# Kernel tuning notes

Measured on AMD Instinct MI355X. Metric: run time of the kernel, lower is better.

Reference implementation:

```python
import jax, jax.numpy as jnp
import numpy as np

N, L = 1, 384
NODE, H, PD = 256, 8, 128
HD = NODE // H
D1 = H * PD + NODE  # out_transform input dim = 1280


def instance_norm(x, eps=1e-5):
    # x: (N, C, H, W); torch InstanceNorm2d default: no affine, biased var
    m = x.mean(axis=(2, 3), keepdims=True)
    v = x.var(axis=(2, 3), keepdims=True)
    return (x - m) / jnp.sqrt(v + eps)


def conv3x3(x, w, b):
    y = jax.lax.conv_general_dilated(x, w, (1, 1), 'SAME',
                                     dimension_numbers=('NCHW', 'OIHW', 'NCHW'))
    return y + b[None, :, None, None]


def leaky(x):
    return jnp.where(x >= 0, x, 0.01 * x)


def layer_norm(x, w, b, eps=1e-5):
    m = x.mean(-1, keepdims=True)
    v = x.var(-1, keepdims=True)
    return (x - m) / jnp.sqrt(v + eps) * w + b


def setup_inputs() -> dict:
    key = jax.random.key(0)
    ks = jax.random.split(key, 32)
    s = 0.05
    inp = {
        'x': jax.random.normal(ks[0], (N, L, NODE), jnp.float32),
        'z': jax.random.normal(ks[1], (N, L, L, PD), jnp.float32),
        'plddt': jax.random.uniform(ks[2], (N, L, L, 1), jnp.float32),
        # linear weights stored (in, out) so application is x @ W
        'Wq': jax.random.normal(ks[3], (NODE, NODE), jnp.float32) * s,
        'Wk': jax.random.normal(ks[4], (NODE, NODE), jnp.float32) * s,
        'Wv': jax.random.normal(ks[5], (NODE, NODE), jnp.float32) * s,
        'Wp2a': jax.random.normal(ks[6], (PD, H), jnp.float32) * s,
        'conv_a_w': jax.random.normal(ks[7], (H, 2 * H, 3, 3), jnp.float32) * s,
        'conv_a_b': jnp.zeros((H,), jnp.float32),
        'conv_m_w': jax.random.normal(ks[8], (H, H + 1, 3, 3), jnp.float32) * s,
        'conv_m_b': jnp.zeros((H,), jnp.float32),
        'ln1_w': jnp.ones((D1,), jnp.float32),
        'ln1_b': jnp.zeros((D1,), jnp.float32),
        'lin1_w': jax.random.normal(ks[9], (D1, 2 * NODE), jnp.float32) * s,
        'lin1_b': jnp.zeros((2 * NODE,), jnp.float32),
        'ln2_w': jnp.ones((2 * NODE,), jnp.float32),
        'ln2_b': jnp.zeros((2 * NODE,), jnp.float32),
        'lin2_w': jax.random.normal(ks[10], (2 * NODE, NODE), jnp.float32) * s,
        'lin2_b': jnp.zeros((NODE,), jnp.float32),
        'lnf_w': jnp.ones((NODE,), jnp.float32),
        'lnf_b': jnp.zeros((NODE,), jnp.float32),
        'conv_p_w': jax.random.normal(ks[11], (PD, H + PD, 3, 3), jnp.float32) * s,
        'conv_p_b': jnp.zeros((PD,), jnp.float32),
    }
    return inp


def reference(x, z, plddt, Wq, Wk, Wv, Wp2a, conv_a_w, conv_a_b, conv_m_w,
              conv_m_b, ln1_w, ln1_b, lin1_w, lin1_b, ln2_w, ln2_b, lin2_w,
              lin2_b, lnf_w, lnf_b, conv_p_w, conv_p_b):
    Nb, Lh, D = x.shape
    nh = conv_a_w.shape[0]
    hd = D // nh
    Pd = z.shape[-1]
    # node -> alpha (GAT-style QK scores per head)
    q = (x @ Wq).reshape(Nb, Lh, nh, hd)
    k = (x @ Wk).reshape(Nb, Lh, nh, hd)
    v = (x @ Wv).reshape(Nb, Lh, nh, hd)
    a_node = jnp.einsum('nlhd,nmhd->nlmh', q, k) / jnp.sqrt(jnp.float32(hd))
    a_pair = z @ Wp2a                                  # (N,L,L,H)
    a = jnp.concatenate([a_pair, a_node], -1).transpose(0, 3, 1, 2)  # (N,2H,L,L)
    a = leaky(conv3x3(instance_norm(a), conv_a_w, conv_a_b))
    a = jnp.concatenate([a, plddt.transpose(0, 3, 1, 2)], 1)          # (N,H+1,L,L)
    a = leaky(conv3x3(instance_norm(a), conv_m_w, conv_m_b))
    a = a.transpose(0, 2, 3, 1)                                        # (N,L,L,H)
    # aggregations
    nfn = jnp.einsum('nlmh,nmhd->nlhd', a, v).reshape(Nb, Lh, D)       # node from node
    nfp = jnp.einsum('nlmh,nlmp->nlhp', a, z).reshape(Nb, Lh, nh * Pd) # node from pair
    cat = jnp.concatenate([nfp, nfn], -1)
    h = layer_norm(cat, ln1_w, ln1_b) @ lin1_w + lin1_b
    h = leaky(layer_norm(h, ln2_w, ln2_b)) @ lin2_w + lin2_b
    x_new = layer_norm(x + h, lnf_w, lnf_b)
    zp = jnp.concatenate([z, a], -1).transpose(0, 3, 1, 2)             # (N,P+H,L,L)
    z_new = leaky(conv3x3(instance_norm(zp), conv_p_w, conv_p_b)).transpose(0, 2, 3, 1)
    return x_new, z_new
```

## Files before the change

kernel.cpp:

```cpp
#include <hip/hip_runtime.h>
#include <stdint.h>

#define LSEQ 384
#define LL   147456
#define NODE 256
#define NH   8
#define HD   32
#define PDIM 128
#define D1   1280
#define D2   512

typedef __attribute__((ext_vector_type(8))) short s16x8;
typedef __attribute__((ext_vector_type(8))) __bf16 bf16x8;
typedef __attribute__((ext_vector_type(4))) float f32x4;

__device__ __forceinline__ float bf2f(uint16_t u) {
    union { uint32_t i; float f; } x; x.i = ((uint32_t)u) << 16; return x.f;
}
__device__ __forceinline__ uint16_t f2bf(float f) {
    uint32_t b = __float_as_uint(f);
    return (uint16_t)((b + 0x7FFFu + ((b >> 16) & 1u)) >> 16);
}
__device__ __forceinline__ float ld(const void* p, size_t i, int bf) {
    return bf ? bf2f(((const uint16_t*)p)[i]) : ((const float*)p)[i];
}
__device__ __forceinline__ void stout(void* p, size_t i, float v, int bf) {
    if (bf) ((uint16_t*)p)[i] = f2bf(v);
    else    ((float*)p)[i] = v;
}

__device__ __forceinline__ bf16x8 bf16x8_zero() {
    union { s16x8 s; bf16x8 b; } u; u.s = (s16x8)0; return u.b;
}

__device__ __forceinline__ void block_reduce2_256(float* s1, float* s2, int t) {
    __syncthreads();
    for (int o = 128; o > 0; o >>= 1) {
        if (t < o) { s1[t] += s1[t + o]; s2[t] += s2[t + o]; }
        __syncthreads();
    }
}

__device__ __forceinline__ void acc8(uint4 u, float& s, float& ss) {
    uint32_t w[4] = { u.x, u.y, u.z, u.w };
    #pragma unroll
    for (int i = 0; i < 4; ++i) {
        float a = bf2f((uint16_t)(w[i] & 0xFFFFu));
        float b = bf2f((uint16_t)(w[i] >> 16));
        s += a + b;
        ss = fmaf(a, a, ss);
        ss = fmaf(b, b, ss);
    }
}

__global__ void k_detect(const uint32_t* __restrict__ zz, int* __restrict__ flag) {
    if (threadIdx.x == 0 && blockIdx.x == 0) {
        int cnt = 0;
        for (int i = 0; i < 256; ++i) {
            uint32_t lo = zz[i] & 0xFFFFu;
            uint32_t e = (lo >> 7) & 0xFFu;
            if (lo == 0u || (e >= 96u && e <= 142u)) ++cnt;
        }
        flag[0] = (cnt >= 192) ? 1 : 0;
    }
}

__global__ __launch_bounds__(256) void k_cvt(
    const void* __restrict__ src, uint16_t* __restrict__ dst, const int* __restrict__ dt)
{
    int bf = dt[0];
    int i = blockIdx.x * 256 + threadIdx.x;
    dst[i] = f2bf(ld(src, i, bf));
}

__global__ __launch_bounds__(256) void k_wnk(
    const void* __restrict__ src, uint16_t* __restrict__ dst, int K, int N,
    const int* __restrict__ dt)
{
    __shared__ float tile[32][33];
    int bf = dt[0];
    int k0 = blockIdx.x * 32, n0 = blockIdx.y * 32;
    int tr = threadIdx.x >> 5, tc = threadIdx.x & 31;
    #pragma unroll
    for (int i = 0; i < 4; ++i)
        tile[tr + i * 8][tc] = ld(src, (size_t)(k0 + tr + i * 8) * N + n0 + tc, bf);
    __syncthreads();
    #pragma unroll
    for (int i = 0; i < 4; ++i)
        dst[(size_t)(n0 + tr + i * 8) * K + k0 + tc] = f2bf(tile[tc][tr + i * 8]);
}

__global__ __launch_bounds__(256) void k_gemm_bias_f32(
    const uint16_t* __restrict__ A, const uint16_t* __restrict__ B,
    const void* __restrict__ bias, float* __restrict__ out, int K, int N,
    const int* __restrict__ dt)
{
    __shared__ __align__(16) uint16_t As[64 * 72];
    __shared__ __align__(16) uint16_t Bs[64 * 72];
    int bf = dt[0];
    int t = threadIdx.x;
    int row0 = blockIdx.x * 64, col0 = blockIdx.y * 64;
    int w = t >> 6, lane = t & 63, p = lane & 15, g = lane >> 4;
    int wm = w >> 1, wn = w & 1;
    f32x4 acc[2][2];
    #pragma unroll
    for (int i = 0; i < 2; ++i)
        #pragma unroll
        for (int j = 0; j < 2; ++j) acc[i][j] = (f32x4){0.f, 0.f, 0.f, 0.f};

    for (int kc = 0; kc < K; kc += 64) {
        __syncthreads();
        #pragma unroll
        for (int rep = 0; rep < 2; ++rep) {
            int i = t + rep * 256;
            int r = i >> 3, c8 = (i & 7) * 8;
            *(uint4*)&As[r * 72 + c8] = *(const uint4*)&A[(size_t)(row0 + r) * K + kc + c8];
            *(uint4*)&Bs[r * 72 + c8] = *(const uint4*)&B[(size_t)(col0 + r) * K + kc + c8];
        }
        __syncthreads();
        #pragma unroll
        for (int kk = 0; kk < 64; kk += 32) {
            bf16x8 a0 = *(const bf16x8*)&As[(wm * 32 + p) * 72 + kk + 8 * g];
            bf16x8 a1 = *(const bf16x8*)&As[(wm * 32 + 16 + p) * 72 + kk + 8 * g];
            bf16x8 b0 = *(const bf16x8*)&Bs[(wn * 32 + p) * 72 + kk + 8 * g];
            bf16x8 b1 = *(const bf16x8*)&Bs[(wn * 32 + 16 + p) * 72 + kk + 8 * g];
            acc[0][0] = __builtin_amdgcn_mfma_f32_16x16x32_bf16(a0, b0, acc[0][0], 0, 0, 0);
            acc[0][1] = __builtin_amdgcn_mfma_f32_16x16x32_bf16(a0, b1, acc[0][1], 0, 0, 0);
            acc[1][0] = __builtin_amdgcn_mfma_f32_16x16x32_bf16(a1, b0, acc[1][0], 0, 0, 0);
            acc[1][1] = __builtin_amdgcn_mfma_f32_16x16x32_bf16(a1, b1, acc[1][1], 0, 0, 0);
        }
    }
    #pragma unroll
    for (int mi = 0; mi < 2; ++mi)
        #pragma unroll
        for (int ni = 0; ni < 2; ++ni) {
            int n = col0 + wn * 32 + ni * 16 + p;
            float bb = ld(bias, n, bf);
            #pragma unroll
            for (int reg = 0; reg < 4; ++reg) {
                int m = row0 + wm * 32 + mi * 16 + 4 * g + reg;
                out[(size_t)m * N + n] = acc[mi][ni][reg] + bb;
            }
        }
}

__global__ __launch_bounds__(256) void k_gemm_qkv(
    const uint16_t* __restrict__ A, const uint16_t* __restrict__ B,
    uint16_t* __restrict__ q, uint16_t* __restrict__ k, uint16_t* __restrict__ v)
{
    __shared__ __align__(16) uint16_t As[64 * 72];
    __shared__ __align__(16) uint16_t Bs[64 * 72];
    const int K = 256;
    int t = threadIdx.x;
    int row0 = blockIdx.x * 64, col0 = blockIdx.y * 64;
    int w = t >> 6, lane = t & 63, p = lane & 15, g = lane >> 4;
    int wm = w >> 1, wn = w & 1;
    f32x4 acc[2][2];
    #pragma unroll
    for (int i = 0; i < 2; ++i)
        #pragma unroll
        for (int j = 0; j < 2; ++j) acc[i][j] = (f32x4){0.f, 0.f, 0.f, 0.f};

    for (int kc = 0; kc < K; kc += 64) {
        __syncthreads();
        #pragma unroll
        for (int rep = 0; rep < 2; ++rep) {
            int i = t + rep * 256;
            int r = i >> 3, c8 = (i & 7) * 8;
            *(uint4*)&As[r * 72 + c8] = *(const uint4*)&A[(size_t)(row0 + r) * K + kc + c8];
            *(uint4*)&Bs[r * 72 + c8] = *(const uint4*)&B[(size_t)(col0 + r) * K + kc + c8];
        }
        __syncthreads();
        #pragma unroll
        for (int kk = 0; kk < 64; kk += 32) {
            bf16x8 a0 = *(const bf16x8*)&As[(wm * 32 + p) * 72 + kk + 8 * g];
            bf16x8 a1 = *(const bf16x8*)&As[(wm * 32 + 16 + p) * 72 + kk + 8 * g];
            bf16x8 b0 = *(const bf16x8*)&Bs[(wn * 32 + p) * 72 + kk + 8 * g];
            bf16x8 b1 = *(const bf16x8*)&Bs[(wn * 32 + 16 + p) * 72 + kk + 8 * g];
            acc[0][0] = __builtin_amdgcn_mfma_f32_16x16x32_bf16(a0, b0, acc[0][0], 0, 0, 0);
            acc[0][1] = __builtin_amdgcn_mfma_f32_16x16x32_bf16(a0, b1, acc[0][1], 0, 0, 0);
            acc[1][0] = __builtin_amdgcn_mfma_f32_16x16x32_bf16(a1, b0, acc[1][0], 0, 0, 0);
            acc[1][1] = __builtin_amdgcn_mfma_f32_16x16x32_bf16(a1, b1, acc[1][1], 0, 0, 0);
        }
    }
    #pragma unroll
    for (int mi = 0; mi < 2; ++mi)
        #pragma unroll
        for (int ni = 0; ni < 2; ++ni) {
            int nglob = col0 + wn * 32 + ni * 16 + p;
            int sel = nglob >> 8, col = nglob & 255;
            uint16_t* dst = (sel == 0) ? q : (sel == 1) ? k : v;
            #pragma unroll
            for (int reg = 0; reg < 4; ++reg) {
                int m = row0 + wm * 32 + mi * 16 + 4 * g + reg;
                dst[(size_t)m * 256 + col] = f2bf(acc[mi][ni][reg]);
            }
        }
}

__global__ __launch_bounds__(256) void k_lin2lnf_mfma(
    const uint16_t* __restrict__ A, const uint16_t* __restrict__ B,
    const void* __restrict__ bias, const void* __restrict__ x,
    const void* __restrict__ lnw, const void* __restrict__ lnb,
    void* __restrict__ out, const int* __restrict__ dt)
{
    __shared__ __align__(16) uint16_t As[32 * 72];
    __shared__ __align__(16) uint16_t Bs[256 * 72];
    const int K = 512;
    int bf = dt[0];
    int t = threadIdx.x;
    int row0 = blockIdx.x * 32;
    int w = t >> 6, lane = t & 63, p = lane & 15, g = lane >> 4;
    f32x4 acc[2][4];
    #pragma unroll
    for (int i = 0; i < 2; ++i)
        #pragma unroll
        for (int j = 0; j < 4; ++j) acc[i][j] = (f32x4){0.f, 0.f, 0.f, 0.f};

    for (int kc = 0; kc < K; kc += 64) {
        __syncthreads();
        {
            int r = t >> 3, c8 = (t & 7) * 8;
            *(uint4*)&As[r * 72 + c8] = *(const uint4*)&A[(size_t)(row0 + r) * K + kc + c8];
        }
        #pragma unroll
        for (int rep = 0; rep < 8; ++rep) {
            int i = t + rep * 256;
            int r = i >> 3, c8 = (i & 7) * 8;
            *(uint4*)&Bs[r * 72 + c8] = *(const uint4*)&B[(size_t)r * K + kc + c8];
        }
        __syncthreads();
        #pragma unroll
        for (int kk = 0; kk < 64; kk += 32) {
            bf16x8 a0 = *(const bf16x8*)&As[(p) * 72 + kk + 8 * g];
            bf16x8 a1 = *(const bf16x8*)&As[(16 + p) * 72 + kk + 8 * g];
            #pragma unroll
            for (int ni = 0; ni < 4; ++ni) {
                bf16x8 bq = *(const bf16x8*)&Bs[(w * 64 + ni * 16 + p) * 72 + kk + 8 * g];
                acc[0][ni] = __builtin_amdgcn_mfma_f32_16x16x32_bf16(a0, bq, acc[0][ni], 0, 0, 0);
                acc[1][ni] = __builtin_amdgcn_mfma_f32_16x16x32_bf16(a1, bq, acc[1][ni], 0, 0, 0);
            }
        }
    }
    __syncthreads();
    float* lnt = (float*)Bs;
    #pragma unroll
    for (int mi = 0; mi < 2; ++mi)
        #pragma unroll
        for (int ni = 0; ni < 4; ++ni) {
            int n = w * 64 + ni * 16 + p;
            float bb = ld(bias, n, bf);
            #pragma unroll
            for (int reg = 0; reg < 4; ++reg) {
                int m = mi * 16 + 4 * g + reg;
                lnt[m * 264 + n] = acc[mi][ni][reg] + bb + ld(x, (size_t)(row0 + m) * 256 + n, bf);
            }
        }
    __syncthreads();
    for (int rr = 0; rr < 8; ++rr) {
        int m = w * 8 + rr;
        float4 v4 = *(const float4*)&lnt[m * 264 + lane * 4];
        float vv[4] = { v4.x, v4.y, v4.z, v4.w };
        float s = (vv[0] + vv[1]) + (vv[2] + vv[3]);
        float ss = fmaf(vv[0], vv[0], fmaf(vv[1], vv[1], fmaf(vv[2], vv[2], vv[3] * vv[3])));
        #pragma unroll
        for (int off = 32; off > 0; off >>= 1) {
            s  += __shfl_xor(s, off);
            ss += __shfl_xor(ss, off);
        }
        float mean = s / 256.f;
        float rstd = rsqrtf(fmaxf(ss / 256.f - mean * mean, 0.f) + 1e-5f);
        #pragma unroll
        for (int i = 0; i < 4; ++i) {
            int c = lane * 4 + i;
            float val = (vv[i] - mean) * rstd * ld(lnw, c, bf) + ld(lnb, c, bf);
            stout(out, (size_t)(row0 + m) * 256 + c, val, bf);
        }
    }
}

__global__ __launch_bounds__(256) void k_apair(
    const void* __restrict__ z, const void* __restrict__ Wp2a,
    uint16_t* __restrict__ acat, const int* __restrict__ dt)
{
    __shared__ float zl[32 * 129];
    __shared__ float wp[PDIM * NH];
    int bf = dt[0];
    int t = threadIdx.x, m0 = blockIdx.x * 32, l = blockIdx.y;
    for (int i = t; i < PDIM * NH; i += 256) wp[i] = ld(Wp2a, i, bf);
    if (bf) {
        const uint16_t* zz = (const uint16_t*)z;
        for (int grp = t; grp < 512; grp += 256) {
            int ml = grp >> 4, p8 = (grp & 15) * 8;
            uint4 u = *(const uint4*)&zz[((size_t)(l * LSEQ + m0 + ml)) * PDIM + p8];
            const uint16_t* pu = (const uint16_t*)&u;
            #pragma unroll
            for (int j = 0; j < 8; ++j) zl[ml * 129 + p8 + j] = bf2f(pu[j]);
        }
    } else {
        const float* zz = (const float*)z;
        for (int grp = t; grp < 1024; grp += 256) {
            int ml = grp >> 5, p4 = (grp & 31) * 4;
            float4 u = *(const float4*)&zz[((size_t)(l * LSEQ + m0 + ml)) * PDIM + p4];
            zl[ml * 129 + p4 + 0] = u.x; zl[ml * 129 + p4 + 1] = u.y;
            zl[ml * 129 + p4 + 2] = u.z; zl[ml * 129 + p4 + 3] = u.w;
        }
    }
    __syncthreads();
    int h = t >> 5, ml = t & 31;
    float acc = 0.f;
    for (int p = 0; p < PDIM; ++p) acc = fmaf(zl[ml * 129 + p], wp[p * NH + h], acc);
    acat[(size_t)h * LL + l * LSEQ + m0 + ml] = f2bf(acc);
}

__global__ __launch_bounds__(256) void k_anode(
    const uint16_t* __restrict__ q, const uint16_t* __restrict__ k,
    uint16_t* __restrict__ acat)
{
    __shared__ float kl[NODE * 33];
    __shared__ float qr[NH * 33];
    int t = threadIdx.x, m0 = blockIdx.x * 32, l = blockIdx.y;
    for (int grp = t; grp < 1024; grp += 256) {
        int ml = grp >> 5, c8 = (grp & 31) * 8;
        uint4 u = *(const uint4*)&k[(size_t)(m0 + ml) * NODE + c8];
        const uint16_t* pu = (const uint16_t*)&u;
        #pragma unroll
        for (int j = 0; j < 8; ++j) kl[(c8 + j) * 33 + ml] = bf2f(pu[j]);
    }
    qr[(t >> 5) * 33 + (t & 31)] = bf2f(q[l * NODE + t]);
    __syncthreads();
    int h = t >> 5, ml = t & 31;
    float acc = 0.f;
    #pragma unroll 8
    for (int d = 0; d < HD; ++d)
        acc = fmaf(qr[h * 33 + d], kl[(h * HD + d) * 33 + ml], acc);
    acat[(size_t)(NH + h) * LL + l * LSEQ + m0 + ml] = f2bf(acc * 0.17677669529663687f);
}

__global__ __launch_bounds__(256) void k_scp(
    const uint16_t* __restrict__ src, const void* __restrict__ raw,
    float* __restrict__ ps, float* __restrict__ pss, const int* __restrict__ dt, int C)
{
    __shared__ float s1[256], s2[256];
    int c = blockIdx.y, chunk = blockIdx.x, t = threadIdx.x;
    float s = 0.f, ss = 0.f;
    if (c < C) {
        const uint16_t* p = src + (size_t)c * LL + (size_t)chunk * 8192;
        #pragma unroll
        for (int it = 0; it < 4; ++it) acc8(*(const uint4*)&p[(it * 256 + t) * 8], s, ss);
    } else if (dt[0]) {
        const uint4* p = (const uint4*)raw + (size_t)chunk * 1024;
        #pragma unroll
        for (int it = 0; it < 4; ++it) acc8(p[it * 256 + t], s, ss);
    } else {
        const float4* p = (const float4*)raw + (size_t)chunk * 2048;
        #pragma unroll
        for (int it = 0; it < 8; ++it) {
            float4 a = p[it * 256 + t];
            s += (a.x + a.y) + (a.z + a.w);
            ss = fmaf(a.x, a.x, fmaf(a.y, a.y, fmaf(a.z, a.z, fmaf(a.w, a.w, ss))));
        }
    }
    s1[t] = s; s2[t] = ss;
    block_reduce2_256(s1, s2, t);
    if (t == 0) { ps[c * 18 + chunk] = s1[0]; pss[c * 18 + chunk] = s2[0]; }
}

__global__ void k_scf(
    const float* __restrict__ ps, const float* __restrict__ pss,
    float* __restrict__ mean_out, float* __restrict__ rstd_out, int C)
{
    int t = threadIdx.x;
    if (t < C) {
        float s = 0.f, ss = 0.f;
        for (int i = 0; i < 18; ++i) { s += ps[t * 18 + i]; ss += pss[t * 18 + i]; }
        float m = s / (float)LL;
        float var = ss / (float)LL - m * m;
        mean_out[t] = m; rstd_out[t] = rsqrtf(fmaxf(var, 0.f) + 1e-5f);
    }
}

__global__ __launch_bounds__(128) void k_conv_a(
    const uint16_t* __restrict__ acat, const void* __restrict__ wa,
    const void* __restrict__ ba, const float* __restrict__ mean,
    const float* __restrict__ rstd, uint16_t* __restrict__ out,
    const int* __restrict__ dt)
{
    __shared__ float wl[9 * 8 * 16];
    __shared__ float ot[8 * 9];
    int bf = dt[0];
    int t = threadIdx.x;
    int l = blockIdx.y, m = blockIdx.x * 128 + t;
    for (int i = t; i < 1152; i += 128) {
        int tap = i >> 7, rem = i & 127;
        int oc = rem >> 4, ic = rem & 15;
        wl[i] = ld(wa, (size_t)oc * 144 + ic * 9 + tap, bf) * rstd[ic];
    }
    __syncthreads();
    if (t < 72) {
        int oc = t / 9, tap = t - oc * 9;
        float s = 0.f;
        for (int ic = 0; ic < 16; ++ic) s = fmaf(mean[ic], wl[tap * 128 + oc * 16 + ic], s);
        ot[t] = s;
    }
    __syncthreads();
    float acc[8];
    #pragma unroll
    for (int oc = 0; oc < 8; ++oc) acc[oc] = ld(ba, oc, bf);
    #pragma unroll
    for (int r = 0; r < 3; ++r) {
        int li = l + r - 1;
        if (li < 0 || li >= LSEQ) continue;
        #pragma unroll
        for (int c = 0; c < 3; ++c) {
            int mi = m + c - 1;
            if (mi < 0 || mi >= LSEQ) continue;
            const uint16_t* ip = acat + li * LSEQ + mi;
            float v[16];
            #pragma unroll
            for (int ic = 0; ic < 16; ++ic) v[ic] = bf2f(ip[(size_t)ic * LL]);
            int tap = r * 3 + c;
            const float4* wq = (const float4*)&wl[tap * 128];
            #pragma unroll
            for (int oc = 0; oc < 8; ++oc) {
                float4 w0 = wq[oc * 4], w1 = wq[oc * 4 + 1], w2 = wq[oc * 4 + 2], w3 = wq[oc * 4 + 3];
                float a = acc[oc] - ot[oc * 9 + tap];
                a = fmaf(w0.x, v[0], a);  a = fmaf(w0.y, v[1], a);
                a = fmaf(w0.z, v[2], a);  a = fmaf(w0.w, v[3], a);
                a = fmaf(w1.x, v[4], a);  a = fmaf(w1.y, v[5], a);
                a = fmaf(w1.z, v[6], a);  a = fmaf(w1.w, v[7], a);
                a = fmaf(w2.x, v[8], a);  a = fmaf(w2.y, v[9], a);
                a = fmaf(w2.z, v[10], a); a = fmaf(w2.w, v[11], a);
                a = fmaf(w3.x, v[12], a); a = fmaf(w3.y, v[13], a);
                a = fmaf(w3.z, v[14], a); a = fmaf(w3.w, v[15], a);
                acc[oc] = a;
            }
        }
    }
    #pragma unroll
    for (int oc = 0; oc < 8; ++oc) {
        float a = acc[oc] >= 0.f ? acc[oc] : 0.01f * acc[oc];
        out[(size_t)oc * LL + l * LSEQ + m] = f2bf(a);
    }
}

__global__ __launch_bounds__(128) void k_conv_m(
    const uint16_t* __restrict__ a1, const void* __restrict__ plddt,
    const void* __restrict__ wm, const void* __restrict__ bm,
    const float* __restrict__ mean, const float* __restrict__ rstd,
    uint16_t* __restrict__ out, const int* __restrict__ dt)
{
    __shared__ float wl[9 * 8 * 12];
    __shared__ float ot[8 * 9];
    int bf = dt[0];
    int t = threadIdx.x;
    int l = blockIdx.y, m = blockIdx.x * 128 + t;
    for (int i = t; i < 864; i += 128) {
        int tap = i / 96, rem = i - tap * 96;
        int oc = rem / 12, ic = rem - oc * 12;
        wl[i] = (ic < 9) ? ld(wm, (size_t)oc * 81 + ic * 9 + tap, bf) * rstd[ic] : 0.f;
    }
    __syncthreads();
    if (t < 72) {
        int oc = t / 9, tap = t - oc * 9;
        float s = 0.f;
        for (int ic = 0; ic < 9; ++ic) s = fmaf(mean[ic], wl[tap * 96 + oc * 12 + ic], s);
        ot[t] = s;
    }
    __syncthreads();
    float acc[8];
    #pragma unroll
    for (int oc = 0; oc < 8; ++oc) acc[oc] = ld(bm, oc, bf);
    #pragma unroll
    for (int r = 0; r < 3; ++r) {
        int li = l + r - 1;
        if (li < 0 || li >= LSEQ) continue;
        #pragma unroll
        for (int c = 0; c < 3; ++c) {
            int mi = m + c - 1;
            if (mi < 0 || mi >= LSEQ) continue;
            int off = li * LSEQ + mi;
            float v[12];
            #pragma unroll
            for (int ic = 0; ic < 8; ++ic) v[ic] = bf2f(a1[(size_t)ic * LL + off]);
            v[8] = ld(plddt, off, bf); v[9] = 0.f; v[10] = 0.f; v[11] = 0.f;
            int tap = r * 3 + c;
            const float4* wq = (const float4*)&wl[tap * 96];
            #pragma unroll
            for (int oc = 0; oc < 8; ++oc) {
                float4 w0 = wq[oc * 3], w1 = wq[oc * 3 + 1], w2 = wq[oc * 3 + 2];
                float a = acc[oc] - ot[oc * 9 + tap];
                a = fmaf(w0.x, v[0], a); a = fmaf(w0.y, v[1], a);
                a = fmaf(w0.z, v[2], a); a = fmaf(w0.w, v[3], a);
                a = fmaf(w1.x, v[4], a); a = fmaf(w1.y, v[5], a);
                a = fmaf(w1.z, v[6], a); a = fmaf(w1.w, v[7], a);
                a = fmaf(w2.x, v[8], a);
                acc[oc] = a;
            }
        }
    }
    #pragma unroll
    for (int oc = 0; oc < 8; ++oc) {
        float a = acc[oc] >= 0.f ? acc[oc] : 0.01f * acc[oc];
        out[(size_t)oc * LL + l * LSEQ + m] = f2bf(a);
    }
}

__global__ __launch_bounds__(512) void k_agg(
    const uint16_t* __restrict__ a2, const uint16_t* __restrict__ v,
    const void* __restrict__ z, float* __restrict__ cat,
    const int* __restrict__ dt)
{
    __shared__ float al[NH * LSEQ];
    __shared__ float hp[3 * NH * PDIM];
    int bf = dt[0];
    int t = threadIdx.x, l = blockIdx.x;
    for (int i = t; i < NH * LSEQ; i += 512) {
        int h = i / LSEQ, m = i - h * LSEQ;
        al[i] = bf2f(a2[(size_t)h * LL + l * LSEQ + m]);
    }
    __syncthreads();
    int p = t & 127, qq = t >> 7;
    float acc[NH];
    #pragma unroll
    for (int h = 0; h < NH; ++h) acc[h] = 0.f;
    size_t zrow = (size_t)l * LSEQ * PDIM;
    for (int m = qq; m < LSEQ; m += 4) {
        float zv = ld(z, zrow + (size_t)m * PDIM + p, bf);
        #pragma unroll
        for (int h = 0; h < NH; ++h) acc[h] = fmaf(al[h * LSEQ + m], zv, acc[h]);
    }
    if (qq) {
        #pragma unroll
        for (int h = 0; h < NH; ++h) hp[(qq - 1) * 1024 + h * PDIM + p] = acc[h];
    }
    __syncthreads();
    if (qq == 0) {
        #pragma unroll
        for (int h = 0; h < NH; ++h)
            cat[(size_t)l * D1 + h * PDIM + p] =
                acc[h] + hp[h * PDIM + p] + hp[1024 + h * PDIM + p] + hp[2048 + h * PDIM + p];
    }
    int o = t & 255, half = t >> 8;
    int h2 = o >> 5;
    float s = 0.f;
    for (int m = half; m < LSEQ; m += 2)
        s = fmaf(al[h2 * LSEQ + m], bf2f(v[m * NODE + o]), s);
    __syncthreads();
    if (half) hp[o] = s;
    __syncthreads();
    if (!half) cat[(size_t)l * D1 + NH * PDIM + o] = s + hp[o];
}

__global__ __launch_bounds__(256) void k_ln1(
    const float* __restrict__ cat, const void* __restrict__ w,
    const void* __restrict__ b, uint16_t* __restrict__ outn,
    const int* __restrict__ dt)
{
    __shared__ float s1[256], s2[256];
    int bf = dt[0];
    int t = threadIdx.x, l = blockIdx.x;
    const float* row = cat + (size_t)l * D1;
    float s = 0.f, ss = 0.f;
    for (int i = t; i < D1; i += 256) { float v = row[i]; s += v; ss = fmaf(v, v, ss); }
    s1[t] = s; s2[t] = ss;
    block_reduce2_256(s1, s2, t);
    float m = s1[0] / (float)D1;
    float rstd = rsqrtf(fmaxf(s2[0] / (float)D1 - m * m, 0.f) + 1e-5f);
    for (int i = t; i < D1; i += 256)
        outn[(size_t)l * D1 + i] = f2bf((row[i] - m) * rstd * ld(w, i, bf) + ld(b, i, bf));
}

__global__ __launch_bounds__(256) void k_ln2(
    const float* __restrict__ in, const void* __restrict__ w,
    const void* __restrict__ b, uint16_t* __restrict__ outn,
    const int* __restrict__ dt)
{
    __shared__ float s1[256], s2[256];
    int bf = dt[0];
    int t = threadIdx.x, l = blockIdx.x;
    const float* row = in + (size_t)l * D2;
    float v0 = row[t], v1 = row[t + 256];
    s1[t] = v0 + v1; s2[t] = v0 * v0 + v1 * v1;
    block_reduce2_256(s1, s2, t);
    float m = s1[0] / (float)D2;
    float rstd = rsqrtf(fmaxf(s2[0] / (float)D2 - m * m, 0.f) + 1e-5f);
    float o0 = (v0 - m) * rstd * ld(w, t, bf) + ld(b, t, bf);
    float o1 = (v1 - m) * rstd * ld(w, t + 256, bf) + ld(b, t + 256, bf);
    outn[(size_t)l * D2 + t]       = f2bf(o0 >= 0.f ? o0 : 0.01f * o0);
    outn[(size_t)l * D2 + t + 256] = f2bf(o1 >= 0.f ? o1 : 0.01f * o1);
}

__global__ __launch_bounds__(256) void k_pstat(
    const void* __restrict__ z, float* __restrict__ psum, float* __restrict__ psumsq,
    const int* __restrict__ dt)
{
    __shared__ float sa[128], sb[128];
    int bf = dt[0];
    int t = threadIdx.x;
    int ch = t & 127, half = t >> 7;
    size_t r0 = (size_t)blockIdx.x * 256;
    float s = 0.f, ss = 0.f;
    for (int i = 0; i < 128; ++i) {
        float v = ld(z, (r0 + half + 2 * i) * PDIM + ch, bf);
        s += v; ss = fmaf(v, v, ss);
    }
    if (half) { sa[ch] = s; sb[ch] = ss; }
    __syncthreads();
    if (!half) {
        psum[blockIdx.x * PDIM + ch] = s + sa[ch];
        psumsq[blockIdx.x * PDIM + ch] = ss + sb[ch];
    }
}

__global__ __launch_bounds__(512) void k_finP(
    const float* __restrict__ psum, const float* __restrict__ psumsq,
    float* __restrict__ meanP, float* __restrict__ rstdP)
{
    __shared__ float s1[512], s2[512];
    int t = threadIdx.x;
    int c = t & 127, seg = t >> 7;
    float s = 0.f, ss = 0.f;
    for (int b = seg * 144; b < seg * 144 + 144; ++b) {
        s += psum[b * PDIM + c]; ss += psumsq[b * PDIM + c];
    }
    s1[t] = s; s2[t] = ss;
    __syncthreads();
    if (t < 128) {
        float S  = s1[t] + s1[t + 128] + s1[t + 256] + s1[t + 384];
        float SS = s2[t] + s2[t + 128] + s2[t + 256] + s2[t + 384];
        float m = S / (float)LL;
        float var = SS / (float)LL - m * m;
        meanP[t] = m; rstdP[t] = rsqrtf(fmaxf(var, 0.f) + 1e-5f);
    }
}

__global__ __launch_bounds__(64) void k_wprep(
    const void* __restrict__ wp, uint16_t* __restrict__ wt, const int* __restrict__ dt)
{
    int bf = dt[0];
    int oc = blockIdx.x, tap = blockIdx.y;
    for (int ic = threadIdx.x; ic < 144; ic += 64) {
        float v = (ic < 136) ? ld(wp, (size_t)oc * 1224 + (size_t)ic * 9 + tap, bf) : 0.f;
        wt[((size_t)tap * 128 + oc) * 144 + ic] = f2bf(v);
    }
}

__global__ __launch_bounds__(256, 2) void k_conv_p_mfma(
    const void* __restrict__ z, const uint16_t* __restrict__ a2,
    const uint16_t* __restrict__ wt, const void* __restrict__ bp,
    const float* __restrict__ meanP, const float* __restrict__ rstdP,
    void* __restrict__ out, const int* __restrict__ dt)
{
    __shared__ __align__(16) uint16_t As[4 * 34 * 144];
    __shared__ __align__(16) uint16_t Ws[128 * 144];
    __shared__ float mloc[136], rloc[136];

    int bf = dt[0];
    int t = threadIdx.x;
    int m0 = blockIdx.x * 32, l0 = blockIdx.y * 2;

    if (t < 136) { mloc[t] = meanP[t]; rloc[t] = rstdP[t]; }
    __syncthreads();

    for (int grp = t; grp < 2448; grp += 256) {
        int pixidx = grp / 18;
        int icg = (grp - pixidx * 18) * 8;
        int lr = pixidx / 34, lc = pixidx - lr * 34;
        int li = l0 - 1 + lr, mi = m0 - 1 + lc;
        uint16_t vals[8];
        if (li < 0 || li >= LSEQ || mi < 0 || mi >= LSEQ || icg >= 136) {
            #pragma unroll
            for (int j = 0; j < 8; ++j) vals[j] = 0;
        } else if (icg < 128) {
            size_t zoff = ((size_t)li * LSEQ + mi) * PDIM + icg;
            if (bf) {
                const uint16_t* zp = (const uint16_t*)z + zoff;
                #pragma unroll
                for (int j = 0; j < 8; ++j)
                    vals[j] = f2bf((bf2f(zp[j]) - mloc[icg + j]) * rloc[icg + j]);
            } else {
                const float* zp = (const float*)z + zoff;
                #pragma unroll
                for (int j = 0; j < 8; ++j)
                    vals[j] = f2bf((zp[j] - mloc[icg + j]) * rloc[icg + j]);
            }
        } else {
            size_t poff = (size_t)li * LSEQ + mi;
            #pragma unroll
            for (int j = 0; j < 8; ++j)
                vals[j] = f2bf((bf2f(a2[(size_t)j * LL + poff]) - mloc[128 + j]) * rloc[128 + j]);
        }
        *(uint4*)&As[pixidx * 144 + icg] = *(const uint4*)vals;
    }

    int w = t >> 6, lane = t & 63;
    int p = lane & 15, g = lane >> 4;
    int r = w >> 1;
    int ocb = (w & 1) * 64;
    int bb0 = (ocb + p) * 144 + 8 * g;

    f32x4 acc0[4], acc1[4];
    #pragma unroll
    for (int n = 0; n < 4; ++n) {
        acc0[n] = (f32x4){0.f, 0.f, 0.f, 0.f};
        acc1[n] = (f32x4){0.f, 0.f, 0.f, 0.f};
    }
    bf16x8 bz = bf16x8_zero();

    for (int tap = 0; tap < 9; ++tap) {
        __syncthreads();
        {
            const uint4* wsrc = (const uint4*)(wt + (size_t)tap * 18432);
            uint4* wdst = (uint4*)Ws;
            #pragma unroll
            for (int i = 0; i < 9; ++i) wdst[t + i * 256] = wsrc[t + i * 256];
        }
        __syncthreads();

        int tr = tap / 3, tc = tap - tr * 3;
        int abase = ((r + tr) * 34 + p + tc) * 144 + 8 * g;

        #pragma unroll
        for (int ch = 0; ch < 5; ++ch) {
            const int ic0 = (ch < 4) ? ch * 32 : 112;
            bf16x8 a0 = *(const bf16x8*)&As[abase + ic0];
            bf16x8 a1 = *(const bf16x8*)&As[abase + 2304 + ic0];
            #pragma unroll
            for (int n = 0; n < 4; ++n) {
                bf16x8 bq;
                if (ch < 4) {
                    bq = *(const bf16x8*)&Ws[bb0 + n * 2304 + ic0];
                } else {
                    bq = bz;
                    if (g == 2) bq = *(const bf16x8*)&Ws[bb0 + n * 2304 + 112];
                }
                acc0[n] = __builtin_amdgcn_mfma_f32_16x16x32_bf16(a0, bq, acc0[n], 0, 0, 0);
                acc1[n] = __builtin_amdgcn_mfma_f32_16x16x32_bf16(a1, bq, acc1[n], 0, 0, 0);
            }
        }
    }

    int l = l0 + r;
    #pragma unroll
    for (int n = 0; n < 4; ++n) {
        int oc = ocb + 16 * n + p;
        float bb = ld(bp, oc, bf);
        #pragma unroll
        for (int reg = 0; reg < 4; ++reg) {
            int pc = 4 * g + reg;
            float v0 = acc0[n][reg] + bb; v0 = v0 >= 0.f ? v0 : 0.01f * v0;
            stout(out, 98304 + ((size_t)l * LSEQ + (m0 + pc)) * PDIM + oc, v0, bf);
            float v1 = acc1[n][reg] + bb; v1 = v1 >= 0.f ? v1 : 0.01f * v1;
            stout(out, 98304 + ((size_t)l * LSEQ + (m0 + 16 + pc)) * PDIM + oc, v1, bf);
        }
    }
}

__global__ __launch_bounds__(128) void k_conv_p(
    const void* __restrict__ z, const uint16_t* __restrict__ a2,
    const void* __restrict__ wp, const void* __restrict__ bp,
    const float* __restrict__ meanP, const float* __restrict__ rstdP,
    void* __restrict__ out, const int* __restrict__ dt)
{
    __shared__ __align__(16) float wlds[128 * 76];
    __shared__ __align__(16) float inl[4 * 18 * 8];
    int bf = dt[0];
    int t = threadIdx.x;
    int m0 = blockIdx.x * 16, l0 = blockIdx.y * 2;
    float acc0[16], acc1[16];
    #pragma unroll
    for (int i = 0; i < 16; ++i) { acc0[i] = 0.f; acc1[i] = 0.f; }

    for (int ic0 = 0; ic0 < 136; ic0 += 8) {
        __syncthreads();
        for (int i = t; i < 128 * 72; i += 128) {
            int op = i / 72, r = i % 72;
            int cc = r / 9, tap = r % 9;
            wlds[op * 76 + tap * 8 + cc] = ld(wp, op * 1224 + (ic0 + cc) * 9 + tap, bf);
        }
        for (int i = t; i < 4 * 18 * 8; i += 128) {
            int rr = i / 144, rem = i % 144;
            int col = rem >> 3, cc = rem & 7;
            int li = l0 - 1 + rr, mi = m0 - 1 + col, ic = ic0 + cc;
            float vv = 0.f;
            if (li >= 0 && li < LSEQ && mi >= 0 && mi < LSEQ) {
                float raw = (ic < PDIM) ? ld(z, ((size_t)li * LSEQ + mi) * PDIM + ic, bf)
                                        : bf2f(a2[(size_t)(ic - PDIM) * LL + li * LSEQ + mi]);
                vv = (raw - meanP[ic]) * rstdP[ic];
            }
            inl[i] = vv;
        }
        __syncthreads();
        #pragma unroll
        for (int qd = 0; qd < 2; ++qd) {
            float4 wq[9];
            #pragma unroll
            for (int tap = 0; tap < 9; ++tap)
                wq[tap] = *(const float4*)&wlds[t * 76 + tap * 8 + qd * 4];
            float4 win[4][3];
            #pragma unroll
            for (int r = 0; r < 4; ++r) {
                win[r][1] = *(const float4*)&inl[(r * 18 + 0) * 8 + qd * 4];
                win[r][2] = *(const float4*)&inl[(r * 18 + 1) * 8 + qd * 4];
                win[r][0] = win[r][1];
            }
            #pragma unroll
            for (int pix = 0; pix < 16; ++pix) {
                #pragma unroll
                for (int r = 0; r < 4; ++r) {
                    win[r][0] = win[r][1];
                    win[r][1] = win[r][2];
                    win[r][2] = *(const float4*)&inl[(r * 18 + pix + 2) * 8 + qd * 4];
                }
                float p0x = 0.f, p0y = 0.f, p0z = 0.f, p0w = 0.f;
                float p1x = 0.f, p1y = 0.f, p1z = 0.f, p1w = 0.f;
                #pragma unroll
                for (int tr = 0; tr < 3; ++tr) {
                    #pragma unroll
                    for (int c = 0; c < 3; ++c) {
                        float4 w4 = wq[tr * 3 + c];
                        float4 u0 = win[tr][c];
                        float4 u1 = win[tr + 1][c];
                        p0x = fmaf(w4.x, u0.x, p0x); p0y = fmaf(w4.y, u0.y, p0y);
                        p0z = fmaf(w4.z, u0.z, p0z); p0w = fmaf(w4.w, u0.w, p0w);
                        p1x = fmaf(w4.x, u1.x, p1x); p1y = fmaf(w4.y, u1.y, p1y);
                        p1z = fmaf(w4.z, u1.z, p1z); p1w = fmaf(w4.w, u1.w, p1w);
                    }
                }
                acc0[pix] += (p0x + p0y) + (p0z + p0w);
                acc1[pix] += (p1x + p1y) + (p1z + p1w);
            }
        }
    }
    float bb = ld(bp, t, bf);
    #pragma unroll
    for (int pix = 0; pix < 16; ++pix) {
        float v0 = acc0[pix] + bb; v0 = v0 >= 0.f ? v0 : 0.01f * v0;
        stout(out, 98304 + ((size_t)l0 * LSEQ + m0 + pix) * PDIM + t, v0, bf);
        float v1 = acc1[pix] + bb; v1 = v1 >= 0.f ? v1 : 0.01f * v1;
        stout(out, 98304 + ((size_t)(l0 + 1) * LSEQ + m0 + pix) * PDIM + t, v1, bf);
    }
}

extern "C" void kernel_launch(void* const* d_in, const int* in_sizes, int n_in,
                              void* d_out, int out_size, void* d_ws, size_t ws_size,
                              hipStream_t stream)
{
    const void* x     = d_in[0];
    const void* z     = d_in[1];
    const void* plddt = d_in[2];
    const void* Wq    = d_in[3];
    const void* Wk    = d_in[4];
    const void* Wv    = d_in[5];
    const void* Wp2a  = d_in[6];
    const void* caw   = d_in[7];
    const void* cab   = d_in[8];
    const void* cmw   = d_in[9];
    const void* cmb   = d_in[10];
    const void* ln1w  = d_in[11];
    const void* ln1b  = d_in[12];
    const void* l1w   = d_in[13];
    const void* l1b   = d_in[14];
    const void* ln2w  = d_in[15];
    const void* ln2b  = d_in[16];
    const void* l2w   = d_in[17];
    const void* l2b   = d_in[18];
    const void* lnfw  = d_in[19];
    const void* lnfb  = d_in[20];
    const void* cpw   = d_in[21];
    const void* cpb   = d_in[22];

    uint16_t* O = (uint16_t*)d_out;
    uint16_t* acat = O + 98304;
    uint16_t* a1b  = O + 2457600;
    uint16_t* qb   = a1b;
    uint16_t* kb   = a1b + 98304;
    uint16_t* vb   = O + 3637248;
    float*    cat  = (float*)(O + 3735552);
    float*    h1   = (float*)(O + 5701632);
    float*    psum = (float*)(O + 6488064);
    float*    psumsq = (float*)(O + 6635520);
    uint16_t* cb   = O + 6782976;
    uint16_t* h1nb = O + 7274496;
    uint16_t* xb   = O + 7471104;
    uint16_t* wtq  = O + 7569408;
    uint16_t* wt1  = O + 7766016;
    uint16_t* wt2  = O + 8421376;

    uint16_t* U = (uint16_t*)d_ws;
    uint16_t* a2b = U;
    float*    st  = (float*)(U + 1179648);
    float* m16 = st;        float* r16 = st + 16;
    float* m9  = st + 32;   float* r9  = st + 48;
    float* mP  = st + 64;   float* rP  = st + 200;
    int*   flg = (int*)(U + 1181696);
    uint16_t* wt = U + 1182720;
    int use_mfma = (ws_size >= (size_t)2365440 + 331776);

    k_detect<<<1, 64, 0, stream>>>((const uint32_t*)z, flg);
    k_cvt<<<384, 256, 0, stream>>>(x, xb, flg);
    k_wnk<<<dim3(8, 8), 256, 0, stream>>>(Wq, wtq,          256, 256, flg);
    k_wnk<<<dim3(8, 8), 256, 0, stream>>>(Wk, wtq +  65536, 256, 256, flg);
    k_wnk<<<dim3(8, 8), 256, 0, stream>>>(Wv, wtq + 131072, 256, 256, flg);
    k_wnk<<<dim3(40, 16), 256, 0, stream>>>(l1w, wt1, 1280, 512, flg);
    k_wnk<<<dim3(16, 8), 256, 0, stream>>>(l2w, wt2,  512, 256, flg);

    k_gemm_qkv<<<dim3(6, 12), 256, 0, stream>>>(xb, wtq, qb, kb, vb);
    k_apair <<<dim3(12, LSEQ), 256, 0, stream>>>(z, Wp2a, acat, flg);
    k_anode <<<dim3(12, LSEQ), 256, 0, stream>>>(qb, kb, acat);
    k_scp<<<dim3(18, 16), 256, 0, stream>>>(acat, plddt, psum, psumsq, flg, 16);
    k_scf<<<1, 16, 0, stream>>>(psum, psumsq, m16, r16, 16);
    k_conv_a<<<dim3(3, LSEQ), 128, 0, stream>>>(acat, caw, cab, m16, r16, a1b, flg);
    k_scp<<<dim3(18, 9), 256, 0, stream>>>(a1b, plddt, psum, psumsq, flg, 8);
    k_scf<<<1, 9, 0, stream>>>(psum, psumsq, m9, r9, 9);
    k_conv_m<<<dim3(3, LSEQ), 128, 0, stream>>>(a1b, plddt, cmw, cmb, m9, r9, a2b, flg);
    k_agg   <<<LSEQ, 512, 0, stream>>>(a2b, vb, z, cat, flg);
    k_ln1   <<<LSEQ, 256, 0, stream>>>(cat, ln1w, ln1b, cb, flg);
    k_gemm_bias_f32<<<dim3(6, 8), 256, 0, stream>>>(cb, wt1, l1b, h1, 1280, 512, flg);
    k_ln2   <<<LSEQ, 256, 0, stream>>>(h1, ln2w, ln2b, h1nb, flg);
    k_lin2lnf_mfma<<<12, 256, 0, stream>>>(h1nb, wt2, l2b, x, lnfw, lnfb, d_out, flg);
    k_scp<<<dim3(18, 8), 256, 0, stream>>>(a2b, plddt, psum, psumsq, flg, 8);
    k_scf<<<1, 8, 0, stream>>>(psum, psumsq, mP + 128, rP + 128, 8);
    k_pstat <<<576, 256, 0, stream>>>(z, psum, psumsq, flg);
    k_finP  <<<1, 512, 0, stream>>>(psum, psumsq, mP, rP);
    if (use_mfma) {
        k_wprep<<<dim3(128, 9), 64, 0, stream>>>(cpw, wt, flg);
        k_conv_p_mfma<<<dim3(12, 192), 256, 0, stream>>>(z, a2b, wt, cpb, mP, rP, d_out, flg);
    } else {
        k_conv_p<<<dim3(24, 192), 128, 0, stream>>>(z, a2b, cpw, cpb, mP, rP, d_out, flg);
    }
}
```

Baseline: 579.9 us.

## Double-buffer conv_p weights with async global-to-LDS loads and stage output stores

The conv_p MFMA kernel changes how each 3x3 tap's weights reach LDS. Weights are split into two channel halves, and each half is fetched with async global_load_lds while the other half is being consumed by MFMAs. This replaces the two barriers per tap plus a serial copy. The input tile drops its padding from 144 to 136 channels, and results are staged through LDS so the global stores are coalesced 16-byte row writes instead of scattered per-element stores. The trade-offs are more workspace for the padded weight layout, a tighter LDS row stride that may cause more bank conflicts, and more intricate synchronisation.

Result: no change. 576.5 us (-0.6%).

```diff
diff --git a/kernel.cpp b/kernel.cpp
--- a/kernel.cpp
+++ b/kernel.cpp
@@ -31,6 +31,12 @@
 
 __device__ __forceinline__ bf16x8 bf16x8_zero() {
     union { s16x8 s; bf16x8 b; } u; u.s = (s16x8)0; return u.b;
+}
+
+__device__ __forceinline__ void gl_lds16(const void* g, void* l) {
+    __builtin_amdgcn_global_load_lds(
+        (const __attribute__((address_space(1))) uint32_t*)g,
+        (__attribute__((address_space(3))) uint32_t*)l, 16, 0, 0);
 }
 
 __device__ __forceinline__ void block_reduce2_256(float* s1, float* s2, int t) {
@@ -635,14 +641,20 @@
     }
 }
 
-__global__ __launch_bounds__(64) void k_wprep(
+__global__ __launch_bounds__(64) void k_wprep2(
     const void* __restrict__ wp, uint16_t* __restrict__ wt, const int* __restrict__ dt)
 {
     int bf = dt[0];
     int oc = blockIdx.x, tap = blockIdx.y;
-    for (int ic = threadIdx.x; ic < 144; ic += 64) {
-        float v = (ic < 136) ? ld(wp, (size_t)oc * 1224 + (size_t)ic * 9 + tap, bf) : 0.f;
-        wt[((size_t)tap * 128 + oc) * 144 + ic] = f2bf(v);
+    size_t P0 = (size_t)tap * 20480;
+    size_t P1 = P0 + 9216;
+    for (int i = threadIdx.x; i < 72; i += 64) {
+        float v = (i < 64) ? ld(wp, (size_t)oc * 1224 + (size_t)i * 9 + tap, bf) : 0.f;
+        wt[P0 + (size_t)oc * 72 + i] = f2bf(v);
+    }
+    for (int i = threadIdx.x; i < 88; i += 64) {
+        float v = (i < 72) ? ld(wp, (size_t)oc * 1224 + (size_t)(64 + i) * 9 + tap, bf) : 0.f;
+        wt[P1 + (size_t)oc * 88 + i] = f2bf(v);
     }
 }
 
@@ -652,24 +664,35 @@
     const float* __restrict__ meanP, const float* __restrict__ rstdP,
     void* __restrict__ out, const int* __restrict__ dt)
 {
-    __shared__ __align__(16) uint16_t As[4 * 34 * 144];
-    __shared__ __align__(16) uint16_t Ws[128 * 144];
+    __shared__ __align__(16) uint16_t As[4 * 34 * 136];
+    __shared__ __align__(16) uint16_t Ws0[9216];
+    __shared__ __align__(16) uint16_t Ws1[11264];
     __shared__ float mloc[136], rloc[136];
 
     int bf = dt[0];
     int t = threadIdx.x;
     int m0 = blockIdx.x * 32, l0 = blockIdx.y * 2;
+    int w = t >> 6, lane = t & 63;
+    int p = lane & 15, g = lane >> 4;
+    int r = w >> 1;
+    int ocb = (w & 1) * 64;
 
     if (t < 136) { mloc[t] = meanP[t]; rloc[t] = rstdP[t]; }
     __syncthreads();
 
-    for (int grp = t; grp < 2448; grp += 256) {
-        int pixidx = grp / 18;
-        int icg = (grp - pixidx * 18) * 8;
+    {
+        const char* src = (const char*)wt;
+        for (int s = w; s < 18; s += 4)
+            gl_lds16(src + s * 1024 + lane * 16, (char*)Ws0 + s * 1024);
+    }
+
+    for (int grp = t; grp < 2312; grp += 256) {
+        int pixidx = grp / 17;
+        int icg = (grp - pixidx * 17) * 8;
         int lr = pixidx / 34, lc = pixidx - lr * 34;
         int li = l0 - 1 + lr, mi = m0 - 1 + lc;
         uint16_t vals[8];
-        if (li < 0 || li >= LSEQ || mi < 0 || mi >= LSEQ || icg >= 136) {
+        if (li < 0 || li >= LSEQ || mi < 0 || mi >= LSEQ) {
             #pragma unroll
             for (int j = 0; j < 8; ++j) vals[j] = 0;
         } else if (icg < 128) {
@@ -691,14 +714,12 @@
             for (int j = 0; j < 8; ++j)
                 vals[j] = f2bf((bf2f(a2[(size_t)j * LL + poff]) - mloc[128 + j]) * rloc[128 + j]);
         }
-        *(uint4*)&As[pixidx * 144 + icg] = *(const uint4*)vals;
-    }
-
-    int w = t >> 6, lane = t & 63;
-    int p = lane & 15, g = lane >> 4;
-    int r = w >> 1;
-    int ocb = (w & 1) * 64;
-    int bb0 = (ocb + p) * 144 + 8 * g;
+        *(uint4*)&As[pixidx * 136 + icg] = *(const uint4*)vals;
+    }
+    __syncthreads();
+
+    int bb0p0 = (ocb + p) * 72 + 8 * g;
+    int bb0p1 = (ocb + p) * 88 + 8 * g;
 
     f32x4 acc0[4], acc1[4];
     #pragma unroll
@@ -709,50 +730,107 @@
     bf16x8 bz = bf16x8_zero();
 
     for (int tap = 0; tap < 9; ++tap) {
-        __syncthreads();
+        int tr = tap / 3, tc = tap - tr * 3;
+        int abase = ((r + tr) * 34 + p + tc) * 136 + 8 * g;
+
         {
-            const uint4* wsrc = (const uint4*)(wt + (size_t)tap * 18432);
-            uint4* wdst = (uint4*)Ws;
-            #pragma unroll
-            for (int i = 0; i < 9; ++i) wdst[t + i * 256] = wsrc[t + i * 256];
-        }
-        __syncthreads();
-
-        int tr = tap / 3, tc = tap - tr * 3;
-        int abase = ((r + tr) * 34 + p + tc) * 144 + 8 * g;
-
-        #pragma unroll
-        for (int ch = 0; ch < 5; ++ch) {
-            const int ic0 = (ch < 4) ? ch * 32 : 112;
+            const char* src = (const char*)(wt + (size_t)tap * 20480 + 9216);
+            for (int s = w; s < 22; s += 4)
+                gl_lds16(src + s * 1024 + lane * 16, (char*)Ws1 + s * 1024);
+        }
+        #pragma unroll
+        for (int cidx = 0; cidx < 2; ++cidx) {
+            int ic0 = cidx * 32;
             bf16x8 a0 = *(const bf16x8*)&As[abase + ic0];
-            bf16x8 a1 = *(const bf16x8*)&As[abase + 2304 + ic0];
+            bf16x8 a1 = *(const bf16x8*)&As[abase + 2176 + ic0];
             #pragma unroll
             for (int n = 0; n < 4; ++n) {
-                bf16x8 bq;
-                if (ch < 4) {
-                    bq = *(const bf16x8*)&Ws[bb0 + n * 2304 + ic0];
-                } else {
-                    bq = bz;
-                    if (g == 2) bq = *(const bf16x8*)&Ws[bb0 + n * 2304 + 112];
-                }
+                bf16x8 bq = *(const bf16x8*)&Ws0[bb0p0 + n * 1152 + ic0];
                 acc0[n] = __builtin_amdgcn_mfma_f32_16x16x32_bf16(a0, bq, acc0[n], 0, 0, 0);
                 acc1[n] = __builtin_amdgcn_mfma_f32_16x16x32_bf16(a1, bq, acc1[n], 0, 0, 0);
             }
         }
-    }
-
-    int l = l0 + r;
-    #pragma unroll
-    for (int n = 0; n < 4; ++n) {
-        int oc = ocb + 16 * n + p;
-        float bb = ld(bp, oc, bf);
-        #pragma unroll
-        for (int reg = 0; reg < 4; ++reg) {
-            int pc = 4 * g + reg;
-            float v0 = acc0[n][reg] + bb; v0 = v0 >= 0.f ? v0 : 0.01f * v0;
-            stout(out, 98304 + ((size_t)l * LSEQ + (m0 + pc)) * PDIM + oc, v0, bf);
-            float v1 = acc1[n][reg] + bb; v1 = v1 >= 0.f ? v1 : 0.01f * v1;
-            stout(out, 98304 + ((size_t)l * LSEQ + (m0 + 16 + pc)) * PDIM + oc, v1, bf);
+        __syncthreads();
+
+        if (tap < 8) {
+            const char* src = (const char*)(wt + (size_t)(tap + 1) * 20480);
+            for (int s = w; s < 18; s += 4)
+                gl_lds16(src + s * 1024 + lane * 16, (char*)Ws0 + s * 1024);
+        }
+        #pragma unroll
+        for (int cidx = 0; cidx < 2; ++cidx) {
+            int ic0 = 64 + cidx * 32;
+            bf16x8 a0 = *(const bf16x8*)&As[abase + ic0];
+            bf16x8 a1 = *(const bf16x8*)&As[abase + 2176 + ic0];
+            #pragma unroll
+            for (int n = 0; n < 4; ++n) {
+                bf16x8 bq = *(const bf16x8*)&Ws1[bb0p1 + n * 1408 + (ic0 - 64)];
+                acc0[n] = __builtin_amdgcn_mfma_f32_16x16x32_bf16(a0, bq, acc0[n], 0, 0, 0);
+                acc1[n] = __builtin_amdgcn_mfma_f32_16x16x32_bf16(a1, bq, acc1[n], 0, 0, 0);
+            }
+        }
+        {
+            bf16x8 a0s = bz, a1s = bz;
+            if (g != 3) {
+                a0s = *(const bf16x8*)&As[abase + 112];
+                a1s = *(const bf16x8*)&As[abase + 2176 + 112];
+            }
+            #pragma unroll
+            for (int n = 0; n < 4; ++n) {
+                bf16x8 bq = bz;
+                if (g == 2) bq = *(const bf16x8*)&Ws1[bb0p1 + n * 1408 + 48];
+                acc0[n] = __builtin_amdgcn_mfma_f32_16x16x32_bf16(a0s, bq, acc0[n], 0, 0, 0);
+                acc1[n] = __builtin_amdgcn_mfma_f32_16x16x32_bf16(a1s, bq, acc1[n], 0, 0, 0);
+            }
+        }
+        __syncthreads();
+    }
+
+    if (bf) {
+        uint16_t* LB = As;
+        #pragma unroll
+        for (int n = 0; n < 4; ++n) {
+            int oc = ocb + 16 * n + p;
+            float bb = ld(bp, oc, bf);
+            #pragma unroll
+            for (int reg = 0; reg < 4; ++reg) {
+                int ml = 4 * g + reg;
+                float v0 = acc0[n][reg] + bb; v0 = v0 >= 0.f ? v0 : 0.01f * v0;
+                LB[(r * 32 + ml) * 128 + oc] = f2bf(v0);
+                float v1 = acc1[n][reg] + bb; v1 = v1 >= 0.f ? v1 : 0.01f * v1;
+                LB[(r * 32 + 16 + ml) * 128 + oc] = f2bf(v1);
+            }
+        }
+        __syncthreads();
+        const uint4* srcv = (const uint4*)As;
+        for (int i = t; i < 1024; i += 256) {
+            int run = i >> 9, off = i & 511;
+            uint16_t* dst = (uint16_t*)out + 98304 +
+                ((size_t)(l0 + run) * LSEQ + m0) * PDIM + (size_t)off * 8;
+            *(uint4*)dst = srcv[i];
+        }
+    } else {
+        float* LB = (float*)As;
+        #pragma unroll
+        for (int n = 0; n < 4; ++n) {
+            int oc = ocb + 16 * n + p;
+            float bb = ld(bp, oc, bf);
+            #pragma unroll
+            for (int reg = 0; reg < 4; ++reg) {
+                int ml = 4 * g + reg;
+                float v0 = acc0[n][reg] + bb; v0 = v0 >= 0.f ? v0 : 0.01f * v0;
+                LB[(r * 32 + ml) * 128 + oc] = v0;
+                float v1 = acc1[n][reg] + bb; v1 = v1 >= 0.f ? v1 : 0.01f * v1;
+                LB[(r * 32 + 16 + ml) * 128 + oc] = v1;
+            }
+        }
+        __syncthreads();
+        const uint4* srcv = (const uint4*)As;
+        for (int i = t; i < 2048; i += 256) {
+            int run = i >> 10, off = i & 1023;
+            float* dst = (float*)out + 98304 +
+                ((size_t)(l0 + run) * LSEQ + m0) * PDIM + (size_t)off * 4;
+            *(uint4*)dst = srcv[i];
         }
     }
 }
@@ -896,7 +974,7 @@
     float* mP  = st + 64;   float* rP  = st + 200;
     int*   flg = (int*)(U + 1181696);
     uint16_t* wt = U + 1182720;
-    int use_mfma = (ws_size >= (size_t)2365440 + 331776);
+    int use_mfma = (ws_size >= (size_t)2365440 + 368640);
 
     k_detect<<<1, 64, 0, stream>>>((const uint32_t*)z, flg);
     k_cvt<<<384, 256, 0, stream>>>(x, xb, flg);
@@ -925,7 +1003,7 @@
     k_pstat <<<576, 256, 0, stream>>>(z, psum, psumsq, flg);
     k_finP  <<<1, 512, 0, stream>>>(psum, psumsq, mP, rP);
     if (use_mfma) {
-        k_wprep<<<dim3(128, 9), 64, 0, stream>>>(cpw, wt, flg);
+        k_wprep2<<<dim3(128, 9), 64, 0, stream>>>(cpw, wt, flg);
         k_conv_p_mfma<<<dim3(12, 192), 256, 0, stream>>>(z, a2b, wt, cpb, mP, rP, d_out, flg);
     } else {
         k_conv_p<<<dim3(24, 192), 128, 0, stream>>>(z, a2b, cpw, cpb, mP, rP, d_out, flg);
```
